# Kernel optimization log

Hardware: AMD Instinct MI355X
Metric: run time of the kernel (lower is better)

The kernel has to match this reference:

```python
import jax, jax.numpy as jnp
import numpy as np

DIM = 256      # dim_hidden * 2
HEADS = 8      # hier_tf_head
C = 256        # out_channels per head (concat=False)
FF = 1024      # dim_hidden * 8
N_HOPS = 4096
HOP_LEN = 12
N_MEM = N_HOPS * HOP_LEN
N = N_HOPS + N_MEM  # 53248 total nodes


def setup_inputs() -> dict:
    key = jax.random.key(0)
    ks = jax.random.split(key, 8)
    x = jax.random.normal(ks[0], (N, DIM), jnp.float32)
    # hop_attn structure built by the python loops: [j,j] self-edges for hop
    # tokens, then one edge (member_node -> hop_token) per member.
    hop_self = np.stack([np.arange(N_HOPS), np.arange(N_HOPS)])
    mem_src = np.arange(N_HOPS, N)
    mem_dst = np.arange(N_MEM) // HOP_LEN
    edge_index = jnp.asarray(
        np.concatenate([hop_self, np.stack([mem_src, mem_dst])], axis=1),
        jnp.int32)  # [2, E]

    def init(k, shp, fan):
        return jax.random.normal(k, shp, jnp.float32) / np.sqrt(fan).astype(np.float32)

    return {
        "x": x,
        "edge_index": edge_index,
        "gat_W": init(ks[1], (DIM, HEADS * C), DIM),
        "gat_att_src": init(ks[2], (HEADS, C), C),
        "gat_att_dst": init(ks[3], (HEADS, C), C),
        "gat_bias": jnp.zeros((C,), jnp.float32),
        "ffn_W1": init(ks[4], (DIM, FF), DIM),
        "ffn_b1": jnp.zeros((FF,), jnp.float32),
        "ffn_W2": init(ks[5], (FF, DIM), FF),
        "ffn_b2": jnp.zeros((DIM,), jnp.float32),
        "ln1_g": jnp.ones((DIM,), jnp.float32),
        "ln1_b": jnp.zeros((DIM,), jnp.float32),
        "ln2_g": jnp.ones((DIM,), jnp.float32),
        "ln2_b": jnp.zeros((DIM,), jnp.float32),
    }


def _layer_norm(x, g, b, eps=1e-5):
    mu = jnp.mean(x, axis=-1, keepdims=True)
    var = jnp.mean(jnp.square(x - mu), axis=-1, keepdims=True)
    return (x - mu) * jax.lax.rsqrt(var + eps) * g + b


def _gat_conv(x, src, dst, W, att_src, att_dst, bias):
    # PyG GATConv, concat=False (mean over heads), negative_slope=0.2
    h = (x @ W).reshape(N, HEADS, C)                       # [N,H,C]
    a_s = jnp.einsum('nhc,hc->nh', h, att_src)             # [N,H]
    a_d = jnp.einsum('nhc,hc->nh', h, att_dst)
    e = jax.nn.leaky_relu(a_s[src] + a_d[dst], 0.2)        # [E,H]
    m = jax.ops.segment_max(e, dst, num_segments=N)        # per-dst softmax
    e = jnp.exp(e - m[dst])
    denom = jax.ops.segment_sum(e, dst, num_segments=N)
    alpha = e / (denom[dst] + 1e-16)                       # [E,H]
    agg = jax.ops.segment_sum(h[src] * alpha[:, :, None], dst, num_segments=N)
    return agg.mean(axis=1) + bias                         # [N,DIM]


def reference(x, edge_index, gat_W, gat_att_src, gat_att_dst, gat_bias,
              ffn_W1, ffn_b1, ffn_W2, ffn_b2, ln1_g, ln1_b, ln2_g, ln2_b):
    # GATConv adds self-loops for every node by default
    loops = jnp.arange(N, dtype=edge_index.dtype)
    src = jnp.concatenate([edge_index[0], loops])
    dst = jnp.concatenate([edge_index[1], loops])
    # GAT + residual + LN (dropout is identity at eval)
    g_out = _gat_conv(x, src, dst, gat_W, gat_att_src, gat_att_dst, gat_bias)
    x1 = _layer_norm(g_out + x, ln1_g, ln1_b)
    # FFN + residual + LN
    ff = jax.nn.relu(x1 @ ffn_W1 + ffn_b1) @ ffn_W2 + ffn_b2
    return _layer_norm(ff + x1, ln2_g, ln2_b)
```

## Files before the change

### kernel.cpp

```cpp
#include <hip/hip_runtime.h>
#include <cstdint>
#include <cstddef>

#define N_TOT   53248
#define N_HOPS  4096
#define HOP_LEN 12
#define NHEAD   8
#define FFD     1024
#define GLD     384

typedef __bf16 bf16x8 __attribute__((ext_vector_type(8)));
typedef float f32x4 __attribute__((ext_vector_type(4)));
typedef float f32x16 __attribute__((ext_vector_type(16)));

__device__ __forceinline__ unsigned short f2bf(float f) {
    unsigned int u = __float_as_uint(f);
    u += 0x7FFFu + ((u >> 16) & 1u);
    return (unsigned short)(u >> 16);
}
__device__ __forceinline__ float bf2f(unsigned short b) {
    return __uint_as_float((unsigned int)b << 16);
}
__device__ __forceinline__ void gload16(const void* g, void* l) {
    __builtin_amdgcn_global_load_lds(
        (const __attribute__((address_space(1))) void*)g,
        (__attribute__((address_space(3))) void*)l, 16, 0, 0);
}

__global__ __launch_bounds__(256) void prep_w(
    const float* __restrict__ W, const float* __restrict__ att_s,
    const float* __restrict__ att_d, unsigned short* __restrict__ BcT)
{
    int d = blockIdx.x, c = threadIdx.x;
    int wave = c >> 6;
    __shared__ float ps4[4], pd4[4];
    float wm = 0.f;
    for (int h = 0; h < NHEAD; ++h) {
        float w = W[d * 2048 + h * 256 + c];
        wm += w;
        float ps = w * att_s[h * 256 + c];
        float pd = w * att_d[h * 256 + c];
        for (int o = 32; o > 0; o >>= 1) {
            ps += __shfl_xor(ps, o);
            pd += __shfl_xor(pd, o);
        }
        if ((c & 63) == 0) { ps4[wave] = ps; pd4[wave] = pd; }
        __syncthreads();
        if (c == 0) BcT[(256 + h) * 256 + d] = f2bf(ps4[0] + ps4[1] + ps4[2] + ps4[3]);
        if (c == 1) BcT[(264 + h) * 256 + d] = f2bf(pd4[0] + pd4[1] + pd4[2] + pd4[3]);
        __syncthreads();
    }
    BcT[c * 256 + d] = f2bf(wm * 0.125f);
}

__global__ __launch_bounds__(256) void tconv(
    const float* __restrict__ in, unsigned short* __restrict__ out,
    int IS, int OS, int in_zoff, int out_zoff)
{
    __shared__ float t[32][33];
    in  += (size_t)blockIdx.z * in_zoff;
    out += (size_t)blockIdx.z * out_zoff;
    int tx = threadIdx.x, ty = threadIdx.y;
    int c0 = blockIdx.x * 32, r0 = blockIdx.y * 32;
    #pragma unroll
    for (int k = 0; k < 4; ++k)
        t[ty + 8 * k][tx] = in[(size_t)(r0 + ty + 8 * k) * IS + c0 + tx];
    __syncthreads();
    #pragma unroll
    for (int k = 0; k < 4; ++k)
        out[(size_t)(c0 + ty + 8 * k) * OS + r0 + tx] = f2bf(t[tx][ty + 8 * k]);
}

__global__ __launch_bounds__(256) void cvt_bf16(
    const float* __restrict__ in, unsigned short* __restrict__ out, int n4)
{
    int i = blockIdx.x * 256 + threadIdx.x;
    if (i >= n4) return;
    float4 v = ((const float4*)in)[i];
    ushort4 o;
    o.x = f2bf(v.x); o.y = f2bf(v.y); o.z = f2bf(v.z); o.w = f2bf(v.w);
    ((ushort4*)out)[i] = o;
}

__global__ __launch_bounds__(256) void hop_z(
    const unsigned short* __restrict__ xb, const unsigned short* __restrict__ gb,
    unsigned short* __restrict__ z)
{
    int j = blockIdx.x, tid = threadIdx.x;
    __shared__ float xr[13][256];
    __shared__ float sm[NHEAD][13];
    __shared__ float walpha[NHEAD][13];
    __shared__ float mxs[NHEAD], invs[NHEAD];

    for (int i = tid; i < 13 * 32; i += 256) {
        int r = i >> 5, c8 = (i & 31) * 8;
        int src = (r == 0) ? j : (N_HOPS + j * HOP_LEN + r - 1);
        uint4 u = *(const uint4*)&xb[(size_t)src * 256 + c8];
        float4 lo, hi;
        lo.x = bf2f((unsigned short)(u.x & 0xFFFF)); lo.y = bf2f((unsigned short)(u.x >> 16));
        lo.z = bf2f((unsigned short)(u.y & 0xFFFF)); lo.w = bf2f((unsigned short)(u.y >> 16));
        hi.x = bf2f((unsigned short)(u.z & 0xFFFF)); hi.y = bf2f((unsigned short)(u.z >> 16));
        hi.z = bf2f((unsigned short)(u.w & 0xFFFF)); hi.w = bf2f((unsigned short)(u.w >> 16));
        *(float4*)&xr[r][c8] = lo;
        *(float4*)&xr[r][c8 + 4] = hi;
    }
    if (tid < NHEAD * 13) {
        int h = tid / 13, k = tid % 13;
        int src = (k == 0) ? j : (N_HOPS + j * HOP_LEN + k - 1);
        float ad = bf2f(gb[(size_t)j * GLD + 264 + h]);
        float v = bf2f(gb[(size_t)src * GLD + 256 + h]) + ad;
        sm[h][k] = v > 0.f ? v : 0.2f * v;
    }
    __syncthreads();
    if (tid < NHEAD) {
        int h = tid;
        float mx = sm[h][0];
        for (int k = 1; k < 13; ++k) mx = fmaxf(mx, sm[h][k]);
        float sum = 2.f * expf(sm[h][0] - mx);
        for (int k = 1; k < 13; ++k) sum += expf(sm[h][k] - mx);
        mxs[h] = mx;
        invs[h] = 0.125f / (sum + 1e-16f);
    }
    __syncthreads();
    if (tid < NHEAD * 13) {
        int h = tid / 13, k = tid % 13;
        walpha[h][k] = (k == 0 ? 2.f : 1.f) * expf(sm[h][k] - mxs[h]) * invs[h];
    }
    __syncthreads();
    for (int h = 0; h < NHEAD; ++h) {
        float acc = 0.f;
        #pragma unroll
        for (int r = 0; r < 13; ++r) acc += walpha[h][r] * xr[r][tid];
        z[((size_t)j * NHEAD + h) * 256 + tid] = f2bf(acc);
    }
}

template <int RELU, int OUT_BF16>
__global__ __launch_bounds__(256) void gemm_bt(
    const unsigned short* __restrict__ A, const unsigned short* __restrict__ BT,
    const float* __restrict__ bias, void* __restrict__ Cout,
    int M, int Nc, int K, int ldc)
{
    __shared__ __align__(16) unsigned short As[128 * 32];
    __shared__ __align__(16) unsigned short Bs[128 * 32];
    const int tid = threadIdx.x;
    const int l = tid & 63;
    const int bm = blockIdx.y * 128, bn = blockIdx.x * 128;
    const int wm = ((tid >> 6) >> 1) * 64, wn = ((tid >> 6) & 1) * 64;

    const int r0 = tid >> 2, ke0 = (tid & 3) * 8;
    const int r1 = (256 + tid) >> 2, ke1 = ((256 + tid) & 3) * 8;
    const unsigned short* ga0 = A + (size_t)(bm + r0) * K + ke0;
    const unsigned short* ga1 = A + (size_t)(bm + r1) * K + ke1;
    const unsigned short* gb0 = BT + (size_t)(bn + r0) * K + ke0;
    const unsigned short* gb1 = BT + (size_t)(bn + r1) * K + ke1;

    f32x4 acc[4][4];
    #pragma unroll
    for (int m = 0; m < 4; ++m)
        #pragma unroll
        for (int n = 0; n < 4; ++n)
            acc[m][n] = (f32x4){0.f, 0.f, 0.f, 0.f};

    const int lrow = l & 15, lk8 = (l >> 4) * 8;

    for (int k0 = 0; k0 < K; k0 += 32) {
        gload16(ga0 + k0, &As[(size_t)tid * 8]);
        gload16(ga1 + k0, &As[(size_t)(256 + tid) * 8]);
        gload16(gb0 + k0, &Bs[(size_t)tid * 8]);
        gload16(gb1 + k0, &Bs[(size_t)(256 + tid) * 8]);
        __syncthreads();
        bf16x8 af[4], bfr[4];
        #pragma unroll
        for (int m = 0; m < 4; ++m)
            af[m] = *(const bf16x8*)&As[(wm + m * 16 + lrow) * 32 + lk8];
        #pragma unroll
        for (int n = 0; n < 4; ++n)
            bfr[n] = *(const bf16x8*)&Bs[(wn + n * 16 + lrow) * 32 + lk8];
        #pragma unroll
        for (int m = 0; m < 4; ++m)
            #pragma unroll
            for (int n = 0; n < 4; ++n)
                acc[m][n] = __builtin_amdgcn_mfma_f32_16x16x32_bf16(
                    af[m], bfr[n], acc[m][n], 0, 0, 0);
        __syncthreads();
    }

    const int orow = (l >> 4) * 4, ocol = l & 15;
    #pragma unroll
    for (int m = 0; m < 4; ++m) {
        int gr = bm + wm + m * 16 + orow;
        #pragma unroll
        for (int n = 0; n < 4; ++n) {
            int gc = bn + wn + n * 16 + ocol;
            float bv = bias[gc];
            #pragma unroll
            for (int r = 0; r < 4; ++r) {
                float v = acc[m][n][r] + bv;
                if (RELU) v = fmaxf(v, 0.f);
                if (OUT_BF16)
                    ((unsigned short*)Cout)[(size_t)(gr + r) * ldc + gc] = f2bf(v);
                else
                    ((float*)Cout)[(size_t)(gr + r) * ldc + gc] = v;
            }
        }
    }
}

__global__ __launch_bounds__(256) void gemm_bt_sk(
    const unsigned short* __restrict__ A, const unsigned short* __restrict__ BT,
    unsigned short* __restrict__ Cpart, int M, int Nc, int Ksl, int ldA)
{
    __shared__ __align__(16) unsigned short As[128 * 32];
    __shared__ __align__(16) unsigned short Bs[128 * 32];
    const int tid = threadIdx.x;
    const int l = tid & 63;
    const int bm = blockIdx.y * 128, bn = blockIdx.x * 128;
    const int koff = blockIdx.z * Ksl;
    const int wm = ((tid >> 6) >> 1) * 64, wn = ((tid >> 6) & 1) * 64;

    const int r0 = tid >> 2, ke0 = (tid & 3) * 8;
    const int r1 = (256 + tid) >> 2, ke1 = ((256 + tid) & 3) * 8;
    const unsigned short* ga0 = A + (size_t)(bm + r0) * ldA + koff + ke0;
    const unsigned short* ga1 = A + (size_t)(bm + r1) * ldA + koff + ke1;
    const unsigned short* gb0 = BT + (size_t)(bn + r0) * ldA + koff + ke0;
    const unsigned short* gb1 = BT + (size_t)(bn + r1) * ldA + koff + ke1;

    f32x4 acc[4][4];
    #pragma unroll
    for (int m = 0; m < 4; ++m)
        #pragma unroll
        for (int n = 0; n < 4; ++n)
            acc[m][n] = (f32x4){0.f, 0.f, 0.f, 0.f};

    const int lrow = l & 15, lk8 = (l >> 4) * 8;

    for (int k0 = 0; k0 < Ksl; k0 += 32) {
        gload16(ga0 + k0, &As[(size_t)tid * 8]);
        gload16(ga1 + k0, &As[(size_t)(256 + tid) * 8]);
        gload16(gb0 + k0, &Bs[(size_t)tid * 8]);
        gload16(gb1 + k0, &Bs[(size_t)(256 + tid) * 8]);
        __syncthreads();
        bf16x8 af[4], bfr[4];
        #pragma unroll
        for (int m = 0; m < 4; ++m)
            af[m] = *(const bf16x8*)&As[(wm + m * 16 + lrow) * 32 + lk8];
        #pragma unroll
        for (int n = 0; n < 4; ++n)
            bfr[n] = *(const bf16x8*)&Bs[(wn + n * 16 + lrow) * 32 + lk8];
        #pragma unroll
        for (int m = 0; m < 4; ++m)
            #pragma unroll
            for (int n = 0; n < 4; ++n)
                acc[m][n] = __builtin_amdgcn_mfma_f32_16x16x32_bf16(
                    af[m], bfr[n], acc[m][n], 0, 0, 0);
        __syncthreads();
    }

    unsigned short* Cp = Cpart + (size_t)blockIdx.z * M * Nc;
    const int orow = (l >> 4) * 4, ocol = l & 15;
    #pragma unroll
    for (int m = 0; m < 4; ++m) {
        int gr = bm + wm + m * 16 + orow;
        #pragma unroll
        for (int n = 0; n < 4; ++n) {
            int gc = bn + wn + n * 16 + ocol;
            #pragma unroll
            for (int r = 0; r < 4; ++r)
                Cp[(size_t)(gr + r) * Nc + gc] = f2bf(acc[m][n][r]);
        }
    }
}

__global__ __launch_bounds__(256) void red_hop(
    const unsigned short* __restrict__ P, const float* __restrict__ bias,
    unsigned short* __restrict__ gbuf)
{
    int i = blockIdx.x * 256 + threadIdx.x;
    int row = i >> 6, c4 = (i & 63) * 4;
    float4 s = { 0.f, 0.f, 0.f, 0.f };
    #pragma unroll
    for (int zz = 0; zz < 8; ++zz) {
        ushort4 u = *(const ushort4*)&P[(size_t)zz * N_HOPS * 256 + (size_t)row * 256 + c4];
        s.x += bf2f(u.x); s.y += bf2f(u.y); s.z += bf2f(u.z); s.w += bf2f(u.w);
    }
    float4 bv = *(const float4*)&bias[c4];
    ushort4 o;
    o.x = f2bf(s.x + bv.x); o.y = f2bf(s.y + bv.y);
    o.z = f2bf(s.z + bv.z); o.w = f2bf(s.w + bv.w);
    *(ushort4*)&gbuf[(size_t)row * GLD + c4] = o;
}

__global__ __launch_bounds__(256) void ln_add_bb(
    const unsigned short* __restrict__ a, const unsigned short* __restrict__ b,
    const float* __restrict__ g, const float* __restrict__ be,
    unsigned short* __restrict__ outp)
{
    int wave = threadIdx.x >> 6, lane = threadIdx.x & 63;
    int n = blockIdx.x * 4 + wave;
    ushort4 av = *(const ushort4*)&a[(size_t)n * GLD + lane * 4];
    ushort4 bv = ((const ushort4*)b)[(size_t)n * 64 + lane];
    float v[4];
    v[0] = bf2f(av.x) + bf2f(bv.x); v[1] = bf2f(av.y) + bf2f(bv.y);
    v[2] = bf2f(av.z) + bf2f(bv.z); v[3] = bf2f(av.w) + bf2f(bv.w);
    float s = v[0] + v[1] + v[2] + v[3];
    for (int o = 32; o > 0; o >>= 1) s += __shfl_xor(s, o);
    float mu = s * (1.f / 256.f);
    float q = 0.f;
    #pragma unroll
    for (int i = 0; i < 4; ++i) { float d = v[i] - mu; q += d * d; }
    for (int o = 32; o > 0; o >>= 1) q += __shfl_xor(q, o);
    float rstd = rsqrtf(q * (1.f / 256.f) + 1e-5f);
    int c = lane * 4;
    float4 gv = *(const float4*)&g[c];
    float4 bev = *(const float4*)&be[c];
    ushort4 o4;
    o4.x = f2bf((v[0] - mu) * rstd * gv.x + bev.x);
    o4.y = f2bf((v[1] - mu) * rstd * gv.y + bev.y);
    o4.z = f2bf((v[2] - mu) * rstd * gv.z + bev.z);
    o4.w = f2bf((v[3] - mu) * rstd * gv.w + bev.w);
    ((ushort4*)outp)[(size_t)n * 64 + lane] = o4;
}

__global__ __launch_bounds__(256, 2) void fused_ffn(
    const unsigned short* __restrict__ x1b, const unsigned short* __restrict__ W1T,
    const float* __restrict__ b1, const unsigned short* __restrict__ W2T,
    const float* __restrict__ b2, const float* __restrict__ g2,
    const float* __restrict__ be2, float* __restrict__ out)
{
    __shared__ __align__(16) char smem[78848];
    unsigned short* sW1u = (unsigned short*)smem;
    unsigned short* sW2u = (unsigned short*)(smem + 32768);
    unsigned short* sHu  = (unsigned short*)(smem + 65536);
    float*          sB1  = (float*)(smem + 74752);

    const int tid = threadIdx.x, l = tid & 63, w = tid >> 6;
    const int l31 = l & 31, h1 = l >> 5;
    const int row0 = blockIdx.x * 64;
    const int rh  = w >> 1;
    const int ch1 = (w & 1) * 32;
    const int hc  = ch1 + l31;

    #pragma unroll
    for (int i = 0; i < 8; ++i) {
        int c = i * 256 + tid;
        int r = c >> 5, s = c & 31;
        gload16(W1T + (size_t)r * 256 + ((s ^ (r & 7)) * 8), sW1u + c * 8);
    }
    #pragma unroll
    for (int i = 0; i < 8; ++i) {
        int c = i * 256 + tid;
        int r = c >> 3, s = c & 7;
        gload16(W2T + (size_t)r * 1024 + ((s ^ (r & 7)) * 8), sW2u + c * 8);
    }
    {
        float4 bv = ((const float4*)b1)[tid];
        *(float4*)&sB1[tid * 4] = bv;
    }
    bf16x8 a[16];
    {
        const unsigned short* xr = x1b + (size_t)(row0 + rh * 32 + l31) * 256 + h1 * 8;
        #pragma unroll
        for (int ks = 0; ks < 16; ++ks)
            a[ks] = *(const bf16x8*)(xr + ks * 16);
    }
    f32x16 facc[2][2];
    #pragma unroll
    for (int m = 0; m < 2; ++m)
        #pragma unroll
        for (int n = 0; n < 2; ++n)
            facc[m][n] = (f32x16)(0.f);
    __syncthreads();

    for (int ch = 0; ch < 16; ++ch) {
        f32x16 hA = (f32x16)(0.f), hB = (f32x16)(0.f);
        #pragma unroll
        for (int ks = 0; ks < 16; ks += 2) {
            bf16x8 w0 = *(const bf16x8*)&sW1u[hc * 256 + (((2 * ks + h1) ^ (hc & 7)) * 8)];
            bf16x8 w1 = *(const bf16x8*)&sW1u[hc * 256 + (((2 * ks + 2 + h1) ^ (hc & 7)) * 8)];
            hA = __builtin_amdgcn_mfma_f32_32x32x16_bf16(a[ks], w0, hA, 0, 0, 0);
            hB = __builtin_amdgcn_mfma_f32_32x32x16_bf16(a[ks + 1], w1, hB, 0, 0, 0);
        }
        float b1v = sB1[ch * 64 + hc];
        #pragma unroll
        for (int reg = 0; reg < 16; ++reg) {
            int r2 = rh * 32 + (reg & 3) + 8 * (reg >> 2) + 4 * h1;
            float v = fmaxf(hA[reg] + hB[reg] + b1v, 0.f);
            sHu[r2 * 72 + hc] = f2bf(v);
        }
        __syncthreads();
        if (ch < 15) {
            #pragma unroll
            for (int i = 0; i < 8; ++i) {
                int c = i * 256 + tid;
                int r = c >> 5, s = c & 31;
                gload16(W1T + (size_t)((ch + 1) * 64 + r) * 256 + ((s ^ (r & 7)) * 8),
                        sW1u + c * 8);
            }
        }
        #pragma unroll
        for (int ks = 0; ks < 4; ++ks) {
            bf16x8 am[2], bn[2];
            #pragma unroll
            for (int m = 0; m < 2; ++m)
                am[m] = *(const bf16x8*)&sHu[(m * 32 + l31) * 72 + (2 * ks + h1) * 8];
            #pragma unroll
            for (int n = 0; n < 2; ++n) {
                int fc = w * 64 + n * 32 + l31;
                bn[n] = *(const bf16x8*)&sW2u[fc * 64 + (((2 * ks + h1) ^ (fc & 7)) * 8)];
            }
            #pragma unroll
            for (int m = 0; m < 2; ++m)
                #pragma unroll
                for (int n = 0; n < 2; ++n)
                    facc[m][n] = __builtin_amdgcn_mfma_f32_32x32x16_bf16(
                        am[m], bn[n], facc[m][n], 0, 0, 0);
        }
        __syncthreads();
        if (ch < 15) {
            #pragma unroll
            for (int i = 0; i < 8; ++i) {
                int c = i * 256 + tid;
                int r = c >> 3, s = c & 7;
                gload16(W2T + (size_t)r * 1024 + (ch + 1) * 64 + ((s ^ (r & 7)) * 8),
                        sW2u + c * 8);
            }
        }
    }

    float b2c[2], g2c[2], be2c[2];
    #pragma unroll
    for (int n = 0; n < 2; ++n) {
        int fc = w * 64 + n * 32 + l31;
        b2c[n] = b2[fc]; g2c[n] = g2[fc]; be2c[n] = be2[fc];
    }
    if ((w & 1) == 0) {
        int r = rh * 32 + l31;
        #pragma unroll
        for (int ks = 0; ks < 16; ++ks)
            *(bf16x8*)&sW1u[r * 256 + (((2 * ks + h1) ^ (r & 7)) * 8)] = a[ks];
    }
    __syncthreads();
    #pragma unroll
    for (int m = 0; m < 2; ++m)
        #pragma unroll
        for (int n = 0; n < 2; ++n)
            #pragma unroll
            for (int reg = 0; reg < 16; ++reg) {
                int r2 = m * 32 + (reg & 3) + 8 * (reg >> 2) + 4 * h1;
                int fc = w * 64 + n * 32 + l31;
                float res = bf2f(sW1u[r2 * 256 + ((((fc >> 3) ^ (r2 & 7)) * 8) | (fc & 7))]);
                facc[m][n][reg] += b2c[n] + res;
            }
    float* lnS = (float*)sW2u;
    float* lnQ = lnS + 256;
    float* lnM = lnQ + 256;
    float* lnR = lnM + 64;
    #pragma unroll
    for (int m = 0; m < 2; ++m)
        #pragma unroll
        for (int reg = 0; reg < 16; ++reg) {
            float s = facc[m][0][reg] + facc[m][1][reg];
            float q = facc[m][0][reg] * facc[m][0][reg]
                    + facc[m][1][reg] * facc[m][1][reg];
            #pragma unroll
            for (int o = 16; o >= 1; o >>= 1) {
                s += __shfl_xor(s, o);
                q += __shfl_xor(q, o);
            }
            if (l31 == 0) {
                int r2 = m * 32 + (reg & 3) + 8 * (reg >> 2) + 4 * h1;
                lnS[r2 * 4 + w] = s;
                lnQ[r2 * 4 + w] = q;
            }
        }
    __syncthreads();
    if (tid < 64) {
        float s = lnS[tid * 4] + lnS[tid * 4 + 1] + lnS[tid * 4 + 2] + lnS[tid * 4 + 3];
        float q = lnQ[tid * 4] + lnQ[tid * 4 + 1] + lnQ[tid * 4 + 2] + lnQ[tid * 4 + 3];
        float mu = s * (1.f / 256.f);
        lnM[tid] = mu;
        lnR[tid] = rsqrtf(q * (1.f / 256.f) - mu * mu + 1e-5f);
    }
    __syncthreads();
    #pragma unroll
    for (int m = 0; m < 2; ++m)
        #pragma unroll
        for (int reg = 0; reg < 16; ++reg) {
            int r2 = m * 32 + (reg & 3) + 8 * (reg >> 2) + 4 * h1;
            float mu = lnM[r2], rs = lnR[r2];
            #pragma unroll
            for (int n = 0; n < 2; ++n) {
                int fc = w * 64 + n * 32 + l31;
                out[(size_t)(row0 + r2) * 256 + fc] =
                    (facc[m][n][reg] - mu) * rs * g2c[n] + be2c[n];
            }
        }
}

extern "C" void kernel_launch(void* const* d_in, const int* in_sizes, int n_in,
                              void* d_out, int out_size, void* d_ws, size_t ws_size,
                              hipStream_t stream)
{
    const float* x       = (const float*)d_in[0];
    const float* gat_W   = (const float*)d_in[2];
    const float* att_src = (const float*)d_in[3];
    const float* att_dst = (const float*)d_in[4];
    const float* gat_b   = (const float*)d_in[5];
    const float* W1      = (const float*)d_in[6];
    const float* b1      = (const float*)d_in[7];
    const float* W2      = (const float*)d_in[8];
    const float* b2      = (const float*)d_in[9];
    const float* ln1_g   = (const float*)d_in[10];
    const float* ln1_b   = (const float*)d_in[11];
    const float* ln2_g   = (const float*)d_in[12];
    const float* ln2_b   = (const float*)d_in[13];
    float* out = (float*)d_out;

    char* p = (char*)d_ws;
    auto carve = [&p](size_t bytes) { char* r = p; p += (bytes + 255) & ~(size_t)255; return r; };
    unsigned short* gbuf = (unsigned short*)carve((size_t)N_TOT * GLD * 2);
    unsigned short* x1b  = (unsigned short*)carve((size_t)N_TOT * 256 * 2);
    unsigned short* z    = (unsigned short*)carve((size_t)N_HOPS * 2048 * 2);
    unsigned short* hopP = (unsigned short*)carve((size_t)8 * N_HOPS * 256 * 2);
    unsigned short* BcT  = (unsigned short*)carve((size_t)GLD * 256 * 2);
    unsigned short* B2T  = (unsigned short*)carve((size_t)2048 * 256 * 2);
    unsigned short* W1T  = (unsigned short*)carve((size_t)FFD * 256 * 2);
    unsigned short* W2T  = (unsigned short*)carve((size_t)256 * FFD * 2);
    float*          bias384 = (float*)carve(GLD * 4);

    hipMemsetAsync(BcT + 272 * 256, 0, (size_t)(GLD - 272) * 256 * 2, stream);
    hipMemcpyAsync(bias384, gat_b, 256 * 4, hipMemcpyDeviceToDevice, stream);
    hipMemsetAsync(bias384 + 256, 0, (GLD - 256) * 4, stream);
    hipLaunchKernelGGL(prep_w, dim3(256), dim3(256), 0, stream,
                       gat_W, att_src, att_dst, BcT);
    hipLaunchKernelGGL(tconv, dim3(8, 8, 8), dim3(32, 8), 0, stream,
                       gat_W, B2T, 2048, 2048, 256, 256);
    hipLaunchKernelGGL(tconv, dim3(32, 8, 1), dim3(32, 8), 0, stream,
                       W1, W1T, 1024, 256, 0, 0);
    hipLaunchKernelGGL(tconv, dim3(8, 32, 1), dim3(32, 8), 0, stream,
                       W2, W2T, 256, 1024, 0, 0);
    hipLaunchKernelGGL(cvt_bf16, dim3(N_TOT * 256 / 4 / 256), dim3(256), 0, stream,
                       x, x1b, N_TOT * 256 / 4);
    hipLaunchKernelGGL((gemm_bt<0, 1>), dim3(GLD / 128, N_TOT / 128), dim3(256), 0, stream,
                       x1b, BcT, bias384, gbuf, N_TOT, GLD, 256, GLD);
    hipLaunchKernelGGL(hop_z, dim3(N_HOPS), dim3(256), 0, stream,
                       x1b, gbuf, z);
    hipLaunchKernelGGL(gemm_bt_sk, dim3(2, N_HOPS / 128, 8), dim3(256), 0, stream,
                       z, B2T, hopP, N_HOPS, 256, 256, 2048);
    hipLaunchKernelGGL(red_hop, dim3(N_HOPS * 64 / 256), dim3(256), 0, stream,
                       hopP, gat_b, gbuf);
    hipLaunchKernelGGL(ln_add_bb, dim3(N_TOT / 4), dim3(256), 0, stream,
                       gbuf, x1b, ln1_g, ln1_b, x1b);
    hipLaunchKernelGGL(fused_ffn, dim3(N_TOT / 64), dim3(256), 0, stream,
                       x1b, W1T, b1, W2T, b2, ln2_g, ln2_b, out);
    (void)in_sizes; (void)n_in; (void)out_size; (void)ws_size;
}
```

Before: 213.0 us.

## Swap MFMA operands in FFN first GEMM for vectorized swizzled hidden stores

The first FFN GEMM now puts the W1 fragment as the A operand and the activations as B, so each lane's accumulator holds consecutive hidden columns. The bias+ReLU output can then be written to LDS as ushort4 vectors into an XOR-swizzled 64-wide layout instead of scalar stores into a padded 72-stride layout. The two split accumulators become one chain, with W1 fragments batched into registers before the MFMAs, and the second GEMM loads two k-steps of operands before issuing its MFMAs. This aims to cut LDS store instructions and bank conflicts, at the cost of a longer serial MFMA dependency chain and more register pressure.

```diff
diff --git a/kernel.cpp b/kernel.cpp
--- a/kernel.cpp
+++ b/kernel.cpp
@@ -328,18 +328,18 @@
     const float* __restrict__ b2, const float* __restrict__ g2,
     const float* __restrict__ be2, float* __restrict__ out)
 {
-    __shared__ __align__(16) char smem[78848];
+    __shared__ __align__(16) char smem[77824];
     unsigned short* sW1u = (unsigned short*)smem;
     unsigned short* sW2u = (unsigned short*)(smem + 32768);
     unsigned short* sHu  = (unsigned short*)(smem + 65536);
-    float*          sB1  = (float*)(smem + 74752);
+    float*          sB1  = (float*)(smem + 73728);
 
     const int tid = threadIdx.x, l = tid & 63, w = tid >> 6;
     const int l31 = l & 31, h1 = l >> 5;
     const int row0 = blockIdx.x * 64;
-    const int rh  = w >> 1;
-    const int ch1 = (w & 1) * 32;
-    const int hc  = ch1 + l31;
+    const int arow = (w & 1) * 32 + l31;
+    const int hcl  = (w >> 1) * 32 + l31;
+    const int hx   = hcl & 7;
 
     #pragma unroll
     for (int i = 0; i < 8; ++i) {
@@ -359,7 +359,7 @@
     }
     bf16x8 a[16];
     {
-        const unsigned short* xr = x1b + (size_t)(row0 + rh * 32 + l31) * 256 + h1 * 8;
+        const unsigned short* xr = x1b + (size_t)(row0 + arow) * 256 + h1 * 8;
         #pragma unroll
         for (int ks = 0; ks < 16; ++ks)
             a[ks] = *(const bf16x8*)(xr + ks * 16);
@@ -373,20 +373,33 @@
     __syncthreads();
 
     for (int ch = 0; ch < 16; ++ch) {
-        f32x16 hA = (f32x16)(0.f), hB = (f32x16)(0.f);
-        #pragma unroll
-        for (int ks = 0; ks < 16; ks += 2) {
-            bf16x8 w0 = *(const bf16x8*)&sW1u[hc * 256 + (((2 * ks + h1) ^ (hc & 7)) * 8)];
-            bf16x8 w1 = *(const bf16x8*)&sW1u[hc * 256 + (((2 * ks + 2 + h1) ^ (hc & 7)) * 8)];
-            hA = __builtin_amdgcn_mfma_f32_32x32x16_bf16(a[ks], w0, hA, 0, 0, 0);
-            hB = __builtin_amdgcn_mfma_f32_32x32x16_bf16(a[ks + 1], w1, hB, 0, 0, 0);
-        }
-        float b1v = sB1[ch * 64 + hc];
-        #pragma unroll
-        for (int reg = 0; reg < 16; ++reg) {
-            int r2 = rh * 32 + (reg & 3) + 8 * (reg >> 2) + 4 * h1;
-            float v = fmaxf(hA[reg] + hB[reg] + b1v, 0.f);
-            sHu[r2 * 72 + hc] = f2bf(v);
+        f32x16 hA = (f32x16)(0.f);
+        {
+            bf16x8 wf[8];
+            #pragma unroll
+            for (int ks = 0; ks < 8; ++ks)
+                wf[ks] = *(const bf16x8*)&sW1u[hcl * 256 + (((2 * ks + h1) ^ hx) * 8)];
+            #pragma unroll
+            for (int ks = 0; ks < 8; ++ks)
+                hA = __builtin_amdgcn_mfma_f32_32x32x16_bf16(wf[ks], a[ks], hA, 0, 0, 0);
+            #pragma unroll
+            for (int ks = 0; ks < 8; ++ks)
+                wf[ks] = *(const bf16x8*)&sW1u[hcl * 256 + (((2 * (ks + 8) + h1) ^ hx) * 8)];
+            #pragma unroll
+            for (int ks = 0; ks < 8; ++ks)
+                hA = __builtin_amdgcn_mfma_f32_32x32x16_bf16(wf[ks], a[ks + 8], hA, 0, 0, 0);
+        }
+        #pragma unroll
+        for (int g = 0; g < 4; ++g) {
+            int hcb = (w >> 1) * 32 + 8 * g + 4 * h1;
+            float4 bv = *(const float4*)&sB1[ch * 64 + hcb];
+            ushort4 o;
+            o.x = f2bf(fmaxf(hA[4 * g + 0] + bv.x, 0.f));
+            o.y = f2bf(fmaxf(hA[4 * g + 1] + bv.y, 0.f));
+            o.z = f2bf(fmaxf(hA[4 * g + 2] + bv.z, 0.f));
+            o.w = f2bf(fmaxf(hA[4 * g + 3] + bv.w, 0.f));
+            int slot = ((w >> 1) * 4 + g) ^ (arow & 7);
+            *(ushort4*)&sHu[arow * 64 + slot * 8 + h1 * 4] = o;
         }
         __syncthreads();
         if (ch < 15) {
@@ -399,22 +412,30 @@
             }
         }
         #pragma unroll
-        for (int ks = 0; ks < 4; ++ks) {
-            bf16x8 am[2], bn[2];
-            #pragma unroll
-            for (int m = 0; m < 2; ++m)
-                am[m] = *(const bf16x8*)&sHu[(m * 32 + l31) * 72 + (2 * ks + h1) * 8];
-            #pragma unroll
-            for (int n = 0; n < 2; ++n) {
-                int fc = w * 64 + n * 32 + l31;
-                bn[n] = *(const bf16x8*)&sW2u[fc * 64 + (((2 * ks + h1) ^ (fc & 7)) * 8)];
-            }
-            #pragma unroll
-            for (int m = 0; m < 2; ++m)
+        for (int kp = 0; kp < 2; ++kp) {
+            bf16x8 am[2][2], bn[2][2];
+            #pragma unroll
+            for (int q = 0; q < 2; ++q) {
+                int ks = kp * 2 + q;
                 #pragma unroll
-                for (int n = 0; n < 2; ++n)
-                    facc[m][n] = __builtin_amdgcn_mfma_f32_32x32x16_bf16(
-                        am[m], bn[n], facc[m][n], 0, 0, 0);
+                for (int m = 0; m < 2; ++m) {
+                    int r = m * 32 + l31;
+                    am[q][m] = *(const bf16x8*)&sHu[r * 64 + (((2 * ks + h1) ^ (r & 7)) * 8)];
+                }
+                #pragma unroll
+                for (int n = 0; n < 2; ++n) {
+                    int fc = w * 64 + n * 32 + l31;
+                    bn[q][n] = *(const bf16x8*)&sW2u[fc * 64 + (((2 * ks + h1) ^ (fc & 7)) * 8)];
+                }
+            }
+            #pragma unroll
+            for (int q = 0; q < 2; ++q)
+                #pragma unroll
+                for (int m = 0; m < 2; ++m)
+                    #pragma unroll
+                    for (int n = 0; n < 2; ++n)
+                        facc[m][n] = __builtin_amdgcn_mfma_f32_32x32x16_bf16(
+                            am[q][m], bn[q][n], facc[m][n], 0, 0, 0);
         }
         __syncthreads();
         if (ch < 15) {
@@ -434,11 +455,10 @@
         int fc = w * 64 + n * 32 + l31;
         b2c[n] = b2[fc]; g2c[n] = g2[fc]; be2c[n] = be2[fc];
     }
-    if ((w & 1) == 0) {
-        int r = rh * 32 + l31;
+    if (w < 2) {
         #pragma unroll
         for (int ks = 0; ks < 16; ++ks)
-            *(bf16x8*)&sW1u[r * 256 + (((2 * ks + h1) ^ (r & 7)) * 8)] = a[ks];
+            *(bf16x8*)&sW1u[arow * 256 + (((2 * ks + h1) ^ (arow & 7)) * 8)] = a[ks];
     }
     __syncthreads();
     #pragma unroll
```

Measured after the change: 215.4 us. Within noise of the previous version (+1.1%).
